# Kernel tuning notes

Hardware: AMD Instinct MI355X
Metric: run time of the kernel (lower is better)

## Reference

```python
import jax, jax.numpy as jnp
import numpy as np
import math

S, B, D = 1024, 8, 1024
H = 16
DK = D // H
F = 4096
EPS = 1e-5


def _layernorm(x, g, b):
    m = jnp.mean(x, axis=-1, keepdims=True)
    v = jnp.mean(jnp.square(x - m), axis=-1, keepdims=True)
    return (x - m) * jax.lax.rsqrt(v + EPS) * g + b


def setup_inputs() -> dict:
    key = jax.random.key(0)
    ks = jax.random.split(key, 16)
    sc = 0.02
    inp = {
        "src": jax.random.normal(ks[0], (S, B, D), dtype=jnp.float32),
        "pos": jax.random.normal(ks[1], (S, B, D), dtype=jnp.float32),
        "Wq": jax.random.normal(ks[2], (D, D), dtype=jnp.float32) * sc,
        "bq": jnp.zeros((D,), dtype=jnp.float32),
        "Wk": jax.random.normal(ks[3], (D, D), dtype=jnp.float32) * sc,
        "bk": jnp.zeros((D,), dtype=jnp.float32),
        "Wv": jax.random.normal(ks[4], (D, D), dtype=jnp.float32) * sc,
        "bv": jnp.zeros((D,), dtype=jnp.float32),
        "Wo": jax.random.normal(ks[5], (D, D), dtype=jnp.float32) * sc,
        "bo": jnp.zeros((D,), dtype=jnp.float32),
        "W1": jax.random.normal(ks[6], (D, F), dtype=jnp.float32) * sc,
        "b1": jnp.zeros((F,), dtype=jnp.float32),
        "W2": jax.random.normal(ks[7], (F, D), dtype=jnp.float32) * sc,
        "b2": jnp.zeros((D,), dtype=jnp.float32),
        "g1": jnp.ones((D,), dtype=jnp.float32),
        "be1": jnp.zeros((D,), dtype=jnp.float32),
        "g2": jnp.ones((D,), dtype=jnp.float32),
        "be2": jnp.zeros((D,), dtype=jnp.float32),
    }
    return inp


def reference(src, pos, Wq, bq, Wk, bk, Wv, bv, Wo, bo, W1, b1, W2, b2, g1, be1, g2, be2):
    # post-norm encoder layer; dropout = identity (eval mode)
    qk_in = src + pos                      # q = k = src + pos, value = src
    # to batch-first [B, S, D]
    qb = jnp.transpose(qk_in, (1, 0, 2))
    vb = jnp.transpose(src, (1, 0, 2))

    def split_heads(x):                    # [B,S,D] -> [B,H,S,DK]
        return jnp.transpose(x.reshape(B, S, H, DK), (0, 2, 1, 3))

    q = split_heads(qb @ Wq + bq)
    k = split_heads(qb @ Wk + bk)
    v = split_heads(vb @ Wv + bv)

    scores = jnp.einsum('bhqd,bhkd->bhqk', q, k) / math.sqrt(DK)
    attn = jax.nn.softmax(scores, axis=-1)             # [B,H,S,S]
    ctx = jnp.einsum('bhqk,bhkd->bhqd', attn, v)       # [B,H,S,DK]
    ctx = jnp.transpose(ctx, (0, 2, 1, 3)).reshape(B, S, D)
    attn_out = ctx @ Wo + bo                           # [B,S,D]
    attn_out = jnp.transpose(attn_out, (1, 0, 2))      # back to [S,B,D]

    x = _layernorm(src + attn_out, g1, be1)
    ffn = jax.nn.relu(x @ W1 + b1) @ W2 + b2
    out = _layernorm(x + ffn, g2, be2)
    return out, attn
```

## Files before the change

kernel.cpp:

```cpp
#include <hip/hip_runtime.h>
#include <stdint.h>

#define S_ 1024
#define B_ 8
#define D_ 1024
#define H_ 16
#define DK_ 64
#define F_ 4096
#define EPS_ 1e-5f

typedef __bf16 bf16_t;
typedef __attribute__((ext_vector_type(8))) __bf16 bf16x8;
typedef __attribute__((ext_vector_type(4))) __bf16 bf16x4;
typedef __attribute__((ext_vector_type(4))) float f32x4;

#define GLD16(gp, lp) __builtin_amdgcn_global_load_lds( \
    (__attribute__((address_space(1))) void*)(void*)(gp), \
    (__attribute__((address_space(3))) void*)(lp), 16, 0, 0)

template<int BM, int BN, int WM, int WN, int MODE>
__global__ __launch_bounds__(256)
void gemm_bt(const bf16_t* __restrict__ A, const bf16_t* __restrict__ Bt,
             const float* __restrict__ bias, void* __restrict__ out,
             int K, int lda, int ldb, int ldc, long batchA, long batchB)
{
    constexpr int MT = WM / 16, NT = WN / 16;
    constexpr int WCOLS = BN / WN;
    __shared__ __align__(16) bf16_t As[BM * 32];
    __shared__ __align__(16) bf16_t Bs[BN * 32];

    const int z = blockIdx.z;
    A += (size_t)z * batchA;
    Bt += (size_t)z * batchB;
    const int rowBase = blockIdx.y * BM;
    const int colBase = blockIdx.x * BN;
    const int tid = threadIdx.x;
    const int wave = tid >> 6, lane = tid & 63;
    const int wr = wave / WCOLS, wc = wave % WCOLS;
    const int lr = lane & 15;
    const int lk = (lane >> 4) * 8;

    f32x4 acc[MT][NT] = {};

    for (int k0 = 0; k0 < K; k0 += 32) {
#pragma unroll
        for (int i = 0; i < BM / 64; ++i) {
            int id = i * 256 + tid;
            GLD16(A + (size_t)(rowBase + (id >> 2)) * lda + k0 + (id & 3) * 8, As + id * 8);
        }
#pragma unroll
        for (int i = 0; i < BN / 64; ++i) {
            int id = i * 256 + tid;
            GLD16(Bt + (size_t)(colBase + (id >> 2)) * ldb + k0 + (id & 3) * 8, Bs + id * 8);
        }
        __syncthreads();
        bf16x8 af[MT], bfr[NT];
#pragma unroll
        for (int mi = 0; mi < MT; ++mi)
            af[mi] = *(const bf16x8*)&As[(wr * WM + mi * 16 + lr) * 32 + lk];
#pragma unroll
        for (int ni = 0; ni < NT; ++ni)
            bfr[ni] = *(const bf16x8*)&Bs[(wc * WN + ni * 16 + lr) * 32 + lk];
#pragma unroll
        for (int mi = 0; mi < MT; ++mi)
#pragma unroll
            for (int ni = 0; ni < NT; ++ni)
                acc[mi][ni] = __builtin_amdgcn_mfma_f32_16x16x32_bf16(af[mi], bfr[ni], acc[mi][ni], 0, 0, 0);
        __syncthreads();
    }

    const int quad = lane >> 4;
#pragma unroll
    for (int mi = 0; mi < MT; ++mi) {
#pragma unroll
        for (int ni = 0; ni < NT; ++ni) {
            const int col = colBase + wc * WN + ni * 16 + lr;
            float bv = 0.f;
            if constexpr (MODE == 0 || MODE == 1 || MODE == 2 || MODE == 3) bv = bias[col];
#pragma unroll
            for (int e = 0; e < 4; ++e) {
                const int row = rowBase + wr * WM + mi * 16 + quad * 4 + e;
                float v = acc[mi][ni][e] + bv;
                if constexpr (MODE == 0) {
                    ((float*)out)[(size_t)row * ldc + col] = v;
                } else if constexpr (MODE == 1) {
                    int s = row >> 3, b = row & 7, h = col >> 6, dk = col & 63;
                    ((bf16_t*)out)[(((size_t)(b * 16 + h) * 1024 + s) << 6) + dk] = (bf16_t)v;
                } else if constexpr (MODE == 2) {
                    int s = row >> 3, b = row & 7, h = col >> 6, dk = col & 63;
                    ((bf16_t*)out)[(((size_t)(b * 16 + h) * 64 + dk) << 10) + s] = (bf16_t)v;
                } else if constexpr (MODE == 3) {
                    ((bf16_t*)out)[(size_t)row * ldc + col] = (bf16_t)fmaxf(v, 0.f);
                }
            }
        }
    }
}

__global__ __launch_bounds__(256)
void fused_attn(const bf16_t* __restrict__ qb, const bf16_t* __restrict__ kb,
                const bf16_t* __restrict__ vt, float* __restrict__ attn,
                bf16_t* __restrict__ ctx)
{
    __shared__ __align__(16) bf16_t Psh[32 * 1024];
    __shared__ float smax[4][32];
    __shared__ float ssum[4][32];

    int flat = blockIdx.y * 32 + blockIdx.x;
    flat = (flat & 7) * 512 + (flat >> 3);
    const int z = flat >> 5;
    const int qBase = (flat & 31) * 32;
    const int b = z >> 4, h = z & 15;
    const int tid = threadIdx.x;
    const int wave = tid >> 6, lane = tid & 63;
    const int lr = lane & 15, quad = lane >> 4;

    const bf16_t* Qz = qb + ((size_t)z << 16);
    const bf16_t* Kz = kb + ((size_t)z << 16);
    const bf16_t* Vz = vt + ((size_t)z << 16);
    float* Az = attn + ((size_t)z << 20);

    bf16x8 qf[2][2];
#pragma unroll
    for (int ni = 0; ni < 2; ++ni)
#pragma unroll
        for (int kk = 0; kk < 2; ++kk)
            qf[ni][kk] = *(const bf16x8*)(Qz + (size_t)(qBase + ni * 16 + lr) * 64 + kk * 32 + quad * 8);

    f32x4 acc[16][2] = {};
#pragma unroll
    for (int mi = 0; mi < 16; ++mi) {
        const bf16_t* kp = Kz + (size_t)(wave * 256 + mi * 16 + lr) * 64 + quad * 8;
        bf16x8 kf0 = *(const bf16x8*)kp;
        bf16x8 kf1 = *(const bf16x8*)(kp + 32);
#pragma unroll
        for (int ni = 0; ni < 2; ++ni) {
            acc[mi][ni] = __builtin_amdgcn_mfma_f32_16x16x32_bf16(kf0, qf[ni][0], acc[mi][ni], 0, 0, 0);
            acc[mi][ni] = __builtin_amdgcn_mfma_f32_16x16x32_bf16(kf1, qf[ni][1], acc[mi][ni], 0, 0, 0);
        }
    }

    float mloc[2];
#pragma unroll
    for (int ni = 0; ni < 2; ++ni) {
        float mx = acc[0][ni][0];
#pragma unroll
        for (int mi = 0; mi < 16; ++mi)
            mx = fmaxf(mx, fmaxf(fmaxf(acc[mi][ni][0], acc[mi][ni][1]),
                                 fmaxf(acc[mi][ni][2], acc[mi][ni][3])));
        mx = fmaxf(mx, __shfl_xor(mx, 16, 64));
        mx = fmaxf(mx, __shfl_xor(mx, 32, 64));
        mloc[ni] = mx;
    }
    if (quad == 0) { smax[wave][lr] = mloc[0]; smax[wave][16 + lr] = mloc[1]; }
    __syncthreads();

    float rs[2];
#pragma unroll
    for (int ni = 0; ni < 2; ++ni) {
        const int qh = ni * 16 + lr;
        const float mm = 0.125f * fmaxf(fmaxf(smax[0][qh], smax[1][qh]),
                                        fmaxf(smax[2][qh], smax[3][qh]));
        float s = 0.f;
#pragma unroll
        for (int mi = 0; mi < 16; ++mi)
#pragma unroll
            for (int e = 0; e < 4; ++e) {
                float p = __expf(fmaf(acc[mi][ni][e], 0.125f, -mm));
                acc[mi][ni][e] = p; s += p;
            }
        s += __shfl_xor(s, 16, 64);
        s += __shfl_xor(s, 32, 64);
        rs[ni] = s;
    }
    if (quad == 0) { ssum[wave][lr] = rs[0]; ssum[wave][16 + lr] = rs[1]; }
    __syncthreads();

#pragma unroll
    for (int ni = 0; ni < 2; ++ni) {
        const int qh = ni * 16 + lr;
        const float r = 1.0f / (ssum[0][qh] + ssum[1][qh] + ssum[2][qh] + ssum[3][qh]);
        float* arow = Az + ((size_t)(qBase + qh) << 10);
#pragma unroll
        for (int mi = 0; mi < 16; ++mi) {
            const int k0 = wave * 256 + mi * 16 + quad * 4;
            float4 o;
            o.x = acc[mi][ni][0] * r; o.y = acc[mi][ni][1] * r;
            o.z = acc[mi][ni][2] * r; o.w = acc[mi][ni][3] * r;
            *(float4*)(arow + k0) = o;
            bf16x4 pb;
            pb[0] = (bf16_t)o.x; pb[1] = (bf16_t)o.y; pb[2] = (bf16_t)o.z; pb[3] = (bf16_t)o.w;
            int byte = qh * 2048 + k0 * 2;
            byte ^= (qh & 7) << 4;
            *(bf16x4*)((char*)Psh + byte) = pb;
        }
    }
    __syncthreads();

    f32x4 cacc[2] = {};
#pragma unroll
    for (int kt = 0; kt < 32; ++kt) {
        bf16x8 vf = *(const bf16x8*)(Vz + (size_t)(wave * 16 + lr) * 1024 + kt * 32 + quad * 8);
#pragma unroll
        for (int mi = 0; mi < 2; ++mi) {
            const int qh = mi * 16 + lr;
            int byte = qh * 2048 + (kt * 32 + quad * 8) * 2;
            byte ^= (qh & 7) << 4;
            bf16x8 af = *(const bf16x8*)((const char*)Psh + byte);
            cacc[mi] = __builtin_amdgcn_mfma_f32_16x16x32_bf16(af, vf, cacc[mi], 0, 0, 0);
        }
    }
#pragma unroll
    for (int mi = 0; mi < 2; ++mi)
#pragma unroll
        for (int e = 0; e < 4; ++e) {
            const int s = qBase + mi * 16 + quad * 4 + e;
            ctx[(((size_t)s * 8 + b) << 10) + h * 64 + wave * 16 + lr] = (bf16_t)cacc[mi][e];
        }
}

__global__ __launch_bounds__(256)
void prep_kernel(const float* __restrict__ src, const float* __restrict__ pos,
                 bf16_t* __restrict__ qk, bf16_t* __restrict__ vv)
{
    const size_t i = ((size_t)blockIdx.x * 256 + threadIdx.x) * 4;
    float4 s = *(const float4*)(src + i);
    float4 q = *(const float4*)(pos + i);
    bf16x4 qo, vo;
    qo[0] = (bf16_t)(s.x + q.x); qo[1] = (bf16_t)(s.y + q.y);
    qo[2] = (bf16_t)(s.z + q.z); qo[3] = (bf16_t)(s.w + q.w);
    vo[0] = (bf16_t)s.x; vo[1] = (bf16_t)s.y; vo[2] = (bf16_t)s.z; vo[3] = (bf16_t)s.w;
    *(bf16x4*)(qk + i) = qo;
    *(bf16x4*)(vv + i) = vo;
}

__global__ __launch_bounds__(256)
void transpose_w(const float* __restrict__ W, bf16_t* __restrict__ WT, int K, int N)
{
    __shared__ float t[32][33];
    const int n0 = blockIdx.x * 32, k0 = blockIdx.y * 32;
    const int tx = threadIdx.x & 31;
    const int ty = threadIdx.x >> 5;
#pragma unroll
    for (int j = 0; j < 32; j += 8)
        t[ty + j][tx] = W[(size_t)(k0 + ty + j) * N + n0 + tx];
    __syncthreads();
#pragma unroll
    for (int j = 0; j < 32; j += 8)
        WT[(size_t)(n0 + ty + j) * K + k0 + tx] = (bf16_t)t[tx][ty + j];
}

__global__ __launch_bounds__(256)
void ln_kernel(const float* __restrict__ a, const float* __restrict__ b,
               const float* __restrict__ g, const float* __restrict__ be,
               float* __restrict__ xf, bf16_t* __restrict__ xb, float* __restrict__ outf)
{
    __shared__ float sh[8];
    const int r = blockIdx.x;
    const int t = threadIdx.x;
    float4 va = ((const float4*)(a + ((size_t)r << 10)))[t];
    float4 vb = ((const float4*)(b + ((size_t)r << 10)))[t];
    float x0 = va.x + vb.x, x1 = va.y + vb.y, x2 = va.z + vb.z, x3 = va.w + vb.w;
    float s = x0 + x1 + x2 + x3;
    float sq = x0 * x0 + x1 * x1 + x2 * x2 + x3 * x3;
#pragma unroll
    for (int o = 32; o > 0; o >>= 1) { s += __shfl_xor(s, o, 64); sq += __shfl_xor(sq, o, 64); }
    const int w = t >> 6, ln = t & 63;
    if (ln == 0) { sh[w] = s; sh[4 + w] = sq; }
    __syncthreads();
    s = sh[0] + sh[1] + sh[2] + sh[3];
    sq = sh[4] + sh[5] + sh[6] + sh[7];
    const float mean = s * (1.f / 1024.f);
    const float var = sq * (1.f / 1024.f) - mean * mean;
    const float rstd = rsqrtf(var + EPS_);
    float4 vg = ((const float4*)g)[t];
    float4 vbe = ((const float4*)be)[t];
    float y0 = (x0 - mean) * rstd * vg.x + vbe.x;
    float y1 = (x1 - mean) * rstd * vg.y + vbe.y;
    float y2 = (x2 - mean) * rstd * vg.z + vbe.z;
    float y3 = (x3 - mean) * rstd * vg.w + vbe.w;
    if (xf) { float4 o4 = {y0, y1, y2, y3}; ((float4*)(xf + ((size_t)r << 10)))[t] = o4; }
    if (xb) {
        bf16x4 ob; ob[0] = (bf16_t)y0; ob[1] = (bf16_t)y1; ob[2] = (bf16_t)y2; ob[3] = (bf16_t)y3;
        ((bf16x4*)(xb + ((size_t)r << 10)))[t] = ob;
    }
    if (outf) { float4 o4 = {y0, y1, y2, y3}; ((float4*)(outf + ((size_t)r << 10)))[t] = o4; }
}

extern "C" void kernel_launch(void* const* d_in, const int* in_sizes, int n_in,
                              void* d_out, int out_size, void* d_ws, size_t ws_size,
                              hipStream_t stream)
{
    (void)in_sizes; (void)n_in; (void)out_size; (void)ws_size;
    const float* src = (const float*)d_in[0];
    const float* pos = (const float*)d_in[1];
    const float* Wq  = (const float*)d_in[2];
    const float* bq  = (const float*)d_in[3];
    const float* Wk  = (const float*)d_in[4];
    const float* bk  = (const float*)d_in[5];
    const float* Wv  = (const float*)d_in[6];
    const float* bv  = (const float*)d_in[7];
    const float* Wo  = (const float*)d_in[8];
    const float* bo  = (const float*)d_in[9];
    const float* W1  = (const float*)d_in[10];
    const float* b1  = (const float*)d_in[11];
    const float* W2  = (const float*)d_in[12];
    const float* b2  = (const float*)d_in[13];
    const float* g1  = (const float*)d_in[14];
    const float* be1 = (const float*)d_in[15];
    const float* g2  = (const float*)d_in[16];
    const float* be2 = (const float*)d_in[17];

    float* outF  = (float*)d_out;
    float* attnF = outF + (size_t)S_ * B_ * D_;

    char* ws = (char*)d_ws;
    size_t off = 0;
    auto alloc = [&](size_t bytes) { void* p = ws + off; off += (bytes + 255) & ~(size_t)255; return p; };

    bf16_t* qk_bf = (bf16_t*)alloc((size_t)8192 * 1024 * 2);
    bf16_t* v_bf  = (bf16_t*)alloc((size_t)8192 * 1024 * 2);
    bf16_t* wqT   = (bf16_t*)alloc((size_t)1024 * 1024 * 2);
    bf16_t* wkT   = (bf16_t*)alloc((size_t)1024 * 1024 * 2);
    bf16_t* wvT   = (bf16_t*)alloc((size_t)1024 * 1024 * 2);
    bf16_t* woT   = (bf16_t*)alloc((size_t)1024 * 1024 * 2);
    bf16_t* w1T   = (bf16_t*)alloc((size_t)4096 * 1024 * 2);
    bf16_t* w2T   = (bf16_t*)alloc((size_t)1024 * 4096 * 2);
    bf16_t* qbuf  = (bf16_t*)alloc((size_t)8 * 16 * 1024 * 64 * 2);
    bf16_t* kbuf  = (bf16_t*)alloc((size_t)8 * 16 * 1024 * 64 * 2);
    bf16_t* vtbuf = (bf16_t*)alloc((size_t)8 * 16 * 64 * 1024 * 2);
    bf16_t* ctx_bf= (bf16_t*)alloc((size_t)8192 * 1024 * 2);
    float*  ao_f  = (float*)alloc((size_t)8192 * 1024 * 4);
    float*  x_f   = (float*)alloc((size_t)8192 * 1024 * 4);
    bf16_t* x_bf  = (bf16_t*)alloc((size_t)8192 * 1024 * 2);
    bf16_t* h_bf  = (bf16_t*)alloc((size_t)8192 * 4096 * 2);
    float*  y_f   = (float*)alloc((size_t)8192 * 1024 * 4);

    transpose_w<<<dim3(32, 32), 256, 0, stream>>>(Wq, wqT, 1024, 1024);
    transpose_w<<<dim3(32, 32), 256, 0, stream>>>(Wk, wkT, 1024, 1024);
    transpose_w<<<dim3(32, 32), 256, 0, stream>>>(Wv, wvT, 1024, 1024);
    transpose_w<<<dim3(32, 32), 256, 0, stream>>>(Wo, woT, 1024, 1024);
    transpose_w<<<dim3(128, 32), 256, 0, stream>>>(W1, w1T, 1024, 4096);
    transpose_w<<<dim3(32, 128), 256, 0, stream>>>(W2, w2T, 4096, 1024);

    prep_kernel<<<8192, 256, 0, stream>>>(src, pos, qk_bf, v_bf);

    gemm_bt<128, 128, 64, 64, 1><<<dim3(8, 64, 1), 256, 0, stream>>>(qk_bf, wqT, bq, qbuf, 1024, 1024, 1024, 0, 0, 0);
    gemm_bt<128, 128, 64, 64, 1><<<dim3(8, 64, 1), 256, 0, stream>>>(qk_bf, wkT, bk, kbuf, 1024, 1024, 1024, 0, 0, 0);
    gemm_bt<128, 128, 64, 64, 2><<<dim3(8, 64, 1), 256, 0, stream>>>(v_bf, wvT, bv, vtbuf, 1024, 1024, 1024, 0, 0, 0);

    fused_attn<<<dim3(32, 128), 256, 0, stream>>>(qbuf, kbuf, vtbuf, attnF, ctx_bf);

    gemm_bt<128, 128, 64, 64, 0><<<dim3(8, 64, 1), 256, 0, stream>>>(ctx_bf, woT, bo, ao_f, 1024, 1024, 1024, 1024, 0, 0);

    ln_kernel<<<8192, 256, 0, stream>>>(src, ao_f, g1, be1, x_f, x_bf, nullptr);

    gemm_bt<128, 128, 64, 64, 3><<<dim3(32, 64, 1), 256, 0, stream>>>(x_bf, w1T, b1, h_bf, 1024, 1024, 1024, 4096, 0, 0);
    gemm_bt<128, 128, 64, 64, 0><<<dim3(8, 64, 1), 256, 0, stream>>>(h_bf, w2T, b2, y_f, 4096, 4096, 4096, 1024, 0, 0);

    ln_kernel<<<8192, 256, 0, stream>>>(x_f, y_f, g2, be2, nullptr, nullptr, outF);
}
```

Before: 699.5 us.

## Add 256x256 eight-wave pipelined GEMM for fused QK projection and FFN1

Introduces gemm8p, a 512-thread GEMM with 256x256 output tiles and double-buffered XOR-swizzled LDS filled by direct global-to-LDS loads. The K loop is hand-interleaved quadrant by quadrant, overlapping loads with MFMA work through explicit waitcnt, barriers and s_setprio. It replaces the two separate Q and K projection launches with one 2048-column launch that writes both head-split outputs, and also replaces the FFN1 ReLU GEMM. The aim is more data reuse per tile and better latency hiding, at the cost of higher register and LDS pressure. The fused QK launch depends on the K weight sitting right after the Q weight in memory.

Result: faster. 654.4 us (-6.4%).

```diff
diff --git a/kernel.cpp b/kernel.cpp
--- a/kernel.cpp
+++ b/kernel.cpp
@@ -17,6 +17,155 @@
 #define GLD16(gp, lp) __builtin_amdgcn_global_load_lds( \
     (__attribute__((address_space(1))) void*)(void*)(gp), \
     (__attribute__((address_space(3))) void*)(lp), 16, 0, 0)
+
+#define BAR() __builtin_amdgcn_s_barrier()
+#define SB0() __builtin_amdgcn_sched_barrier(0)
+#define LG0() do { asm volatile("s_waitcnt lgkmcnt(0)" ::: "memory"); SB0(); } while (0)
+#define VM6() asm volatile("s_waitcnt vmcnt(6)" ::: "memory")
+
+template<int MODE>
+__global__ __launch_bounds__(512, 2)
+void gemm8p(const bf16_t* __restrict__ A, const bf16_t* __restrict__ Bt,
+            const float* __restrict__ bias, const float* __restrict__ bias2,
+            void* __restrict__ out, void* __restrict__ out2,
+            int K, int lda, int ldb, int ldc)
+{
+    __shared__ __align__(16) bf16_t AsL[2][256][64];
+    __shared__ __align__(16) bf16_t BsL[2][256][64];
+
+    const int nwg = gridDim.x * gridDim.y;
+    int flat = blockIdx.y * gridDim.x + blockIdx.x;
+    flat = (flat & 7) * (nwg >> 3) + (flat >> 3);
+    const int bx = flat % gridDim.x, by = flat / gridDim.x;
+    const int rowBase = by * 256, colBase = bx * 256;
+
+    const int tid = threadIdx.x;
+    const int lane = tid & 63;
+    const int wave = tid >> 6;
+    const int wr = wave >> 2, wc = wave & 3;
+    const int lr = lane & 15, quad = lane >> 4;
+
+    const int r0 = tid >> 3, r1 = 64 + r0;
+    const int cs = (tid & 7) ^ (r0 & 7);
+    const int cl = tid & 7;
+    const bf16_t* a0p = A + (size_t)(rowBase + r0) * lda + cs * 8;
+    const bf16_t* a1p = A + (size_t)(rowBase + r1) * lda + cs * 8;
+    const bf16_t* b0p = Bt + (size_t)(colBase + r0) * ldb + cs * 8;
+    const bf16_t* b1p = Bt + (size_t)(colBase + r1) * ldb + cs * 8;
+
+#define STAGE_A(buf, h, kel) do { \
+    GLD16(a0p + (size_t)(h) * 128 * lda + (kel), &AsL[buf][(h) * 128 + r0][cl * 8]); \
+    GLD16(a1p + (size_t)(h) * 128 * lda + (kel), &AsL[buf][(h) * 128 + r1][cl * 8]); } while (0)
+#define STAGE_B(buf, h, kel) do { \
+    GLD16(b0p + (size_t)(h) * 128 * ldb + (kel), &BsL[buf][(h) * 128 + r0][cl * 8]); \
+    GLD16(b1p + (size_t)(h) * 128 * ldb + (kel), &BsL[buf][(h) * 128 + r1][cl * 8]); } while (0)
+
+#define RDA(buf, qm, AF) do { \
+    _Pragma("unroll") for (int mi = 0; mi < 4; ++mi) { \
+        const int r_ = (qm) * 128 + wr * 64 + mi * 16 + lr; \
+        _Pragma("unroll") for (int kk = 0; kk < 2; ++kk) \
+            AF[mi * 2 + kk] = *(const bf16x8*)&AsL[buf][r_][((kk * 4 + quad) ^ (lr & 7)) * 8]; } } while (0)
+#define RDB(buf, qn, BF) do { \
+    _Pragma("unroll") for (int ni = 0; ni < 2; ++ni) { \
+        const int r_ = (qn) * 128 + wc * 32 + ni * 16 + lr; \
+        _Pragma("unroll") for (int kk = 0; kk < 2; ++kk) \
+            BF[ni * 2 + kk] = *(const bf16x8*)&BsL[buf][r_][((kk * 4 + quad) ^ (lr & 7)) * 8]; } } while (0)
+
+#define MQ(qm, qn, AF, BF) do { \
+    __builtin_amdgcn_s_setprio(1); \
+    _Pragma("unroll") for (int kk = 0; kk < 2; ++kk) \
+    _Pragma("unroll") for (int mi = 0; mi < 4; ++mi) \
+    _Pragma("unroll") for (int ni = 0; ni < 2; ++ni) \
+        acc[(qm) * 4 + mi][(qn) * 2 + ni] = __builtin_amdgcn_mfma_f32_16x16x32_bf16( \
+            AF[mi * 2 + kk], BF[ni * 2 + kk], acc[(qm) * 4 + mi][(qn) * 2 + ni], 0, 0, 0); \
+    __builtin_amdgcn_s_setprio(0); } while (0)
+
+    f32x4 acc[8][4] = {};
+    bf16x8 af[8], bq0[4], bq1[4];
+
+    STAGE_A(0, 0, 0); STAGE_B(0, 0, 0); STAGE_B(0, 1, 0); STAGE_A(0, 1, 0);
+    STAGE_A(1, 0, 64); STAGE_B(1, 0, 64); STAGE_B(1, 1, 64);
+    VM6();
+    BAR(); SB0();
+
+    const int NT = K >> 6;
+    const int kCap = K - 64;
+    for (int it = 0; it < (NT >> 1); ++it) {
+        const int kP1 = it * 128 + 64;
+        int kN0 = it * 128 + 128; if (kN0 > kCap) kN0 = kCap;
+        int kN1 = it * 128 + 192; if (kN1 > kCap) kN1 = kCap;
+
+        RDA(0, 0, af); RDB(0, 0, bq0);
+        STAGE_A(1, 1, kP1);
+        BAR(); LG0();
+        MQ(0, 0, af, bq0);
+        BAR(); SB0();
+        RDB(0, 1, bq1);
+        STAGE_A(0, 0, kN0);
+        BAR(); LG0();
+        MQ(0, 1, af, bq1);
+        BAR(); SB0();
+        RDA(0, 1, af);
+        STAGE_B(0, 0, kN0);
+        BAR(); LG0();
+        MQ(1, 1, af, bq1);
+        BAR(); SB0();
+        STAGE_B(0, 1, kN0);
+        BAR(); SB0();
+        MQ(1, 0, af, bq0);
+        VM6();
+        BAR(); SB0();
+        RDA(1, 0, af); RDB(1, 0, bq0);
+        STAGE_A(0, 1, kN0);
+        BAR(); LG0();
+        MQ(0, 0, af, bq0);
+        BAR(); SB0();
+        RDB(1, 1, bq1);
+        STAGE_A(1, 0, kN1);
+        BAR(); LG0();
+        MQ(0, 1, af, bq1);
+        BAR(); SB0();
+        RDA(1, 1, af);
+        STAGE_B(1, 0, kN1);
+        BAR(); LG0();
+        MQ(1, 1, af, bq1);
+        BAR(); SB0();
+        STAGE_B(1, 1, kN1);
+        BAR(); SB0();
+        MQ(1, 0, af, bq0);
+        VM6();
+        BAR(); SB0();
+    }
+
+#pragma unroll
+    for (int mi = 0; mi < 8; ++mi) {
+#pragma unroll
+        for (int ni = 0; ni < 4; ++ni) {
+            const int col = colBase + (ni >> 1) * 128 + wc * 32 + (ni & 1) * 16 + lr;
+            float bv;
+            if constexpr (MODE == 0) bv = (col < 1024) ? bias[col] : bias2[col - 1024];
+            else bv = bias[col];
+#pragma unroll
+            for (int e = 0; e < 4; ++e) {
+                const int row = rowBase + (mi >> 2) * 128 + wr * 64 + (mi & 3) * 16 + quad * 4 + e;
+                const float v = acc[mi][ni][e] + bv;
+                if constexpr (MODE == 0) {
+                    const int sel = col >> 10, c10 = col & 1023;
+                    const int s = row >> 3, b = row & 7, h = c10 >> 6, dk = c10 & 63;
+                    bf16_t* dst = sel ? (bf16_t*)out2 : (bf16_t*)out;
+                    dst[(((size_t)(b * 16 + h) * 1024 + s) << 6) + dk] = (bf16_t)v;
+                } else {
+                    ((bf16_t*)out)[(size_t)row * ldc + col] = (bf16_t)fmaxf(v, 0.f);
+                }
+            }
+        }
+    }
+#undef STAGE_A
+#undef STAGE_B
+#undef RDA
+#undef RDB
+#undef MQ
+}
 
 template<int BM, int BN, int WM, int WN, int MODE>
 __global__ __launch_bounds__(256)
@@ -75,22 +224,16 @@
 #pragma unroll
         for (int ni = 0; ni < NT; ++ni) {
             const int col = colBase + wc * WN + ni * 16 + lr;
-            float bv = 0.f;
-            if constexpr (MODE == 0 || MODE == 1 || MODE == 2 || MODE == 3) bv = bias[col];
+            float bv = bias[col];
 #pragma unroll
             for (int e = 0; e < 4; ++e) {
                 const int row = rowBase + wr * WM + mi * 16 + quad * 4 + e;
                 float v = acc[mi][ni][e] + bv;
                 if constexpr (MODE == 0) {
                     ((float*)out)[(size_t)row * ldc + col] = v;
-                } else if constexpr (MODE == 1) {
-                    int s = row >> 3, b = row & 7, h = col >> 6, dk = col & 63;
-                    ((bf16_t*)out)[(((size_t)(b * 16 + h) * 1024 + s) << 6) + dk] = (bf16_t)v;
                 } else if constexpr (MODE == 2) {
                     int s = row >> 3, b = row & 7, h = col >> 6, dk = col & 63;
                     ((bf16_t*)out)[(((size_t)(b * 16 + h) * 64 + dk) << 10) + s] = (bf16_t)v;
-                } else if constexpr (MODE == 3) {
-                    ((bf16_t*)out)[(size_t)row * ldc + col] = (bf16_t)fmaxf(v, 0.f);
                 }
             }
         }
@@ -345,8 +488,7 @@
 
     prep_kernel<<<8192, 256, 0, stream>>>(src, pos, qk_bf, v_bf);
 
-    gemm_bt<128, 128, 64, 64, 1><<<dim3(8, 64, 1), 256, 0, stream>>>(qk_bf, wqT, bq, qbuf, 1024, 1024, 1024, 0, 0, 0);
-    gemm_bt<128, 128, 64, 64, 1><<<dim3(8, 64, 1), 256, 0, stream>>>(qk_bf, wkT, bk, kbuf, 1024, 1024, 1024, 0, 0, 0);
+    gemm8p<0><<<dim3(8, 32), 512, 0, stream>>>(qk_bf, wqT, bq, bk, qbuf, kbuf, 1024, 1024, 1024, 0);
     gemm_bt<128, 128, 64, 64, 2><<<dim3(8, 64, 1), 256, 0, stream>>>(v_bf, wvT, bv, vtbuf, 1024, 1024, 1024, 0, 0, 0);
 
     fused_attn<<<dim3(32, 128), 256, 0, stream>>>(qbuf, kbuf, vtbuf, attnF, ctx_bf);
@@ -355,7 +497,7 @@
 
     ln_kernel<<<8192, 256, 0, stream>>>(src, ao_f, g1, be1, x_f, x_bf, nullptr);
 
-    gemm_bt<128, 128, 64, 64, 3><<<dim3(32, 64, 1), 256, 0, stream>>>(x_bf, w1T, b1, h_bf, 1024, 1024, 1024, 4096, 0, 0);
+    gemm8p<1><<<dim3(16, 32), 512, 0, stream>>>(x_bf, w1T, b1, nullptr, h_bf, nullptr, 1024, 1024, 1024, 4096);
     gemm_bt<128, 128, 64, 64, 0><<<dim3(8, 64, 1), 256, 0, stream>>>(h_bf, w2T, b2, y_f, 4096, 4096, 4096, 1024, 0, 0);
 
     ln_kernel<<<8192, 256, 0, stream>>>(x_f, y_f, g2, be2, nullptr, nullptr, outF);
```
